# Kernel optimization log

Hardware: AMD Instinct MI355X
Metric: run time of the kernel (lower is better)

The kernel has to match this reference:

```python
import jax, jax.numpy as jnp
import numpy as np

K = 5
P = 1.5
MU = 0.01
N_NODES = 100000
N_EDGES = 1600000
D_FEAT = 32


def setup_inputs() -> dict:
    key = jax.random.key(0)
    k1, k2 = jax.random.split(key)
    h = jax.random.normal(k1, (N_NODES, D_FEAT), dtype=jnp.float32)
    edge_index = jax.random.randint(k2, (2, N_EDGES), 0, N_NODES, dtype=jnp.int64)
    return {"h": h, "edge_index": edge_index}


def reference(h, edge_index):
    row, col = edge_index[0], edge_index[1]
    for _ in range(K):
        diff = h[row] - h[col]                      # [E, d] gather
        norm_diff = jnp.maximum(jnp.linalg.norm(diff, axis=1), 1e-6)  # [E]
        weights = (norm_diff / norm_diff.max()) ** (P - 2.0)          # [E]
        # agg[r] += sum over edges with row==r of weights * (h[col] - h[row])
        msgs = weights[:, None] * (-diff)           # [E, d]
        agg = jax.ops.segment_sum(msgs, row, num_segments=N_NODES)    # [N, d]
        h = h - MU * agg
    return h
```

## Files before the change

kernel.cpp:

```cpp
#include <hip/hip_runtime.h>

#define NN 100000
#define NE 1600000
#define DF 32
#define KIT 5
#define MU 0.01f
#define NSLOT 256
#define NV4 (NN * DF / 4)
#define ELLW 36
#define AUXCAP 65536
#define NSLICE 8
#define SLICEN (NN / NSLICE)


__global__ __launch_bounds__(256) void zero_kernel(int* __restrict__ p, int n) {
    int i = blockIdx.x * blockDim.x + threadIdx.x;
    if (i < n) p[i] = 0;
}

__global__ __launch_bounds__(256) void ell_fill_kernel(const int* __restrict__ row,
                                                       const int* __restrict__ col,
                                                       int* __restrict__ degc,
                                                       int* __restrict__ colell,
                                                       int* __restrict__ auxcnt,
                                                       int2* __restrict__ aux) {
    const int slice = blockIdx.x & (NSLICE - 1);
    const int group = blockIdx.x >> 3;
    const int ngroups = gridDim.x >> 3;
    const int lo = slice * SLICEN;
    const int hi = lo + SLICEN;
    for (int e = group * 256 + (int)threadIdx.x; e < NE; e += ngroups * 256) {
        const int r = row[e];
        if (r >= lo && r < hi) {
            const int c = col[e];
            const int pos = atomicAdd(&degc[r], 1);
            if (pos < ELLW) {
                colell[r * ELLW + pos] = c;
            } else {
                const int a = atomicAdd(auxcnt, 1);
                if (a < AUXCAP) aux[a] = make_int2(r, c);
            }
        }
    }
}


__device__ __forceinline__ unsigned int pack2bf(float a, float b) {
    unsigned int ua = __float_as_uint(a);
    unsigned int ub = __float_as_uint(b);
    return ((ua + 0x8000u) >> 16) | (((ub + 0x8000u) >> 16) << 16);
}

__device__ __forceinline__ void unpack8(uint4 v, float* f) {
    f[0] = __uint_as_float(v.x << 16);
    f[1] = __uint_as_float(v.x & 0xffff0000u);
    f[2] = __uint_as_float(v.y << 16);
    f[3] = __uint_as_float(v.y & 0xffff0000u);
    f[4] = __uint_as_float(v.z << 16);
    f[5] = __uint_as_float(v.z & 0xffff0000u);
    f[6] = __uint_as_float(v.w << 16);
    f[7] = __uint_as_float(v.w & 0xffff0000u);
}

__global__ __launch_bounds__(256) void tobf16_kernel(const float4* __restrict__ h,
                                                     uint2* __restrict__ hb) {
    int i = blockIdx.x * blockDim.x + threadIdx.x;
    if (i < NV4) {
        const float4 v = h[i];
        hb[i] = make_uint2(pack2bf(v.x, v.y), pack2bf(v.z, v.w));
    }
}


__global__ __launch_bounds__(256) void agg_kernel(const uint4* __restrict__ hb4,
                                                  const int* __restrict__ degc,
                                                  const int* __restrict__ colell,
                                                  float* __restrict__ S,
                                                  int* __restrict__ maxslots) {
    const int lane = threadIdx.x & 31;
    const int q = lane >> 2;
    const int f2 = lane & 3;
    const int pair = (blockIdx.x * blockDim.x + threadIdx.x) >> 5;
    const int n0 = pair * 2;
    const int n1 = n0 + 1;

    const int d0 = min(degc[n0], ELLW);
    const int d1 = min(degc[n1], ELLW);

    const int ca = (lane < d0) ? colell[n0 * ELLW + lane] : n0;
    const int cb = (lane < d1) ? colell[n1 * ELLW + lane] : n1;
    const uint4 hru0 = hb4[n0 * 4 + f2];
    const uint4 hru1 = hb4[n1 * 4 + f2];

    uint4 u0[4], u1[4];
    #pragma unroll
    for (int j = 0; j < 4; ++j) u0[j] = hb4[__shfl(ca, 8 * j + q, 32) * 4 + f2];
    #pragma unroll
    for (int j = 0; j < 4; ++j) u1[j] = hb4[__shfl(cb, 8 * j + q, 32) * 4 + f2];

    float hr0[8], hr1[8];
    unpack8(hru0, hr0);
    unpack8(hru1, hr1);

    float acc0[8], acc1[8];
    #pragma unroll
    for (int i = 0; i < 8; ++i) { acc0[i] = 0.0f; acc1[i] = 0.0f; }
    float nmax = 0.0f;

    #pragma unroll
    for (int j = 0; j < 4; ++j) {
        float d[8];
        unpack8(u0[j], d);
        float s = 0.0f;
        #pragma unroll
        for (int i = 0; i < 8; ++i) {
            d[i] = hr0[i] - d[i];
            s = fmaf(d[i], d[i], s);
        }
        s += __shfl_xor(s, 1, 32);
        s += __shfl_xor(s, 2, 32);
        const float n = fmaxf(sqrtf(s), 1e-6f);
        nmax = fmaxf(nmax, n);
        const float w = rsqrtf(n);
        #pragma unroll
        for (int i = 0; i < 8; ++i) acc0[i] = fmaf(-d[i], w, acc0[i]);
    }
    #pragma unroll
    for (int j = 0; j < 4; ++j) {
        float d[8];
        unpack8(u1[j], d);
        float s = 0.0f;
        #pragma unroll
        for (int i = 0; i < 8; ++i) {
            d[i] = hr1[i] - d[i];
            s = fmaf(d[i], d[i], s);
        }
        s += __shfl_xor(s, 1, 32);
        s += __shfl_xor(s, 2, 32);
        const float n = fmaxf(sqrtf(s), 1e-6f);
        nmax = fmaxf(nmax, n);
        const float w = rsqrtf(n);
        #pragma unroll
        for (int i = 0; i < 8; ++i) acc1[i] = fmaf(-d[i], w, acc1[i]);
    }

    for (int k = 32; k < d0; k += 8) {
        const int ei = k + q;
        const int c = (ei < d0) ? colell[n0 * ELLW + ei] : n0;
        const uint4 uu = hb4[c * 4 + f2];
        float d[8];
        unpack8(uu, d);
        float s = 0.0f;
        #pragma unroll
        for (int i = 0; i < 8; ++i) {
            d[i] = hr0[i] - d[i];
            s = fmaf(d[i], d[i], s);
        }
        s += __shfl_xor(s, 1, 32);
        s += __shfl_xor(s, 2, 32);
        const float n = fmaxf(sqrtf(s), 1e-6f);
        nmax = fmaxf(nmax, n);
        const float w = rsqrtf(n);
        #pragma unroll
        for (int i = 0; i < 8; ++i) acc0[i] = fmaf(-d[i], w, acc0[i]);
    }
    for (int k = 32; k < d1; k += 8) {
        const int ei = k + q;
        const int c = (ei < d1) ? colell[n1 * ELLW + ei] : n1;
        const uint4 uu = hb4[c * 4 + f2];
        float d[8];
        unpack8(uu, d);
        float s = 0.0f;
        #pragma unroll
        for (int i = 0; i < 8; ++i) {
            d[i] = hr1[i] - d[i];
            s = fmaf(d[i], d[i], s);
        }
        s += __shfl_xor(s, 1, 32);
        s += __shfl_xor(s, 2, 32);
        const float n = fmaxf(sqrtf(s), 1e-6f);
        nmax = fmaxf(nmax, n);
        const float w = rsqrtf(n);
        #pragma unroll
        for (int i = 0; i < 8; ++i) acc1[i] = fmaf(-d[i], w, acc1[i]);
    }

    #pragma unroll
    for (int m = 4; m < 32; m <<= 1) {
        #pragma unroll
        for (int i = 0; i < 8; ++i) {
            acc0[i] += __shfl_xor(acc0[i], m, 32);
            acc1[i] += __shfl_xor(acc1[i], m, 32);
        }
    }
    if (q == 0) {
        ((float4*)S)[n0 * 8 + f2 * 2] = make_float4(acc0[0], acc0[1], acc0[2], acc0[3]);
        ((float4*)S)[n0 * 8 + f2 * 2 + 1] = make_float4(acc0[4], acc0[5], acc0[6], acc0[7]);
        ((float4*)S)[n1 * 8 + f2 * 2] = make_float4(acc1[0], acc1[1], acc1[2], acc1[3]);
        ((float4*)S)[n1 * 8 + f2 * 2 + 1] = make_float4(acc1[4], acc1[5], acc1[6], acc1[7]);
    }

    nmax = fmaxf(nmax, __shfl_xor(nmax, 4, 32));
    nmax = fmaxf(nmax, __shfl_xor(nmax, 8, 32));
    nmax = fmaxf(nmax, __shfl_xor(nmax, 16, 32));
    nmax = fmaxf(nmax, __shfl_xor(nmax, 32, 64));
    if ((threadIdx.x & 63) == 0) {
        atomicMax(&maxslots[blockIdx.x & (NSLOT - 1)], __float_as_int(nmax));
    }
}

__global__ __launch_bounds__(256) void aux_kernel(const uint2* __restrict__ hb,
                                                  const int2* __restrict__ aux,
                                                  const int* __restrict__ auxcnt,
                                                  float* __restrict__ S,
                                                  int* __restrict__ maxslots) {
    const int n = min(*auxcnt, AUXCAP);
    for (int i = blockIdx.x * blockDim.x + threadIdx.x; i < n;
         i += gridDim.x * blockDim.x) {
        const int r = aux[i].x;
        const int c = aux[i].y;
        float d[32];
        float s = 0.0f;
        for (int j = 0; j < 8; ++j) {
            const uint2 ur = hb[r * 8 + j];
            const uint2 uc = hb[c * 8 + j];
            float fr[4], fc[4];
            fr[0] = __uint_as_float(ur.x << 16);
            fr[1] = __uint_as_float(ur.x & 0xffff0000u);
            fr[2] = __uint_as_float(ur.y << 16);
            fr[3] = __uint_as_float(ur.y & 0xffff0000u);
            fc[0] = __uint_as_float(uc.x << 16);
            fc[1] = __uint_as_float(uc.x & 0xffff0000u);
            fc[2] = __uint_as_float(uc.y << 16);
            fc[3] = __uint_as_float(uc.y & 0xffff0000u);
            #pragma unroll
            for (int k = 0; k < 4; ++k) {
                d[j * 4 + k] = fr[k] - fc[k];
                s = fmaf(d[j * 4 + k], d[j * 4 + k], s);
            }
        }
        const float nn = fmaxf(sqrtf(s), 1e-6f);
        atomicMax(&maxslots[i & (NSLOT - 1)], __float_as_int(nn));
        const float w = rsqrtf(nn);
        for (int f = 0; f < 32; ++f) atomicAdd(&S[r * DF + f], -d[f] * w);
    }
}

__global__ __launch_bounds__(256) void update_kernel(const float4* __restrict__ hcur,
                                                     float4* __restrict__ hnxt,
                                                     uint2* __restrict__ hb,
                                                     const float4* __restrict__ S,
                                                     const int* __restrict__ slots) {
    const int t = threadIdx.x;
    int v = slots[t];
    #pragma unroll
    for (int m = 32; m > 0; m >>= 1) v = max(v, __shfl_xor(v, m, 64));
    __shared__ int sm[4];
    __shared__ float sscale;
    if ((t & 63) == 0) sm[t >> 6] = v;
    __syncthreads();
    if (t == 0) {
        int bm = max(max(sm[0], sm[1]), max(sm[2], sm[3]));
        sscale = MU * sqrtf(__int_as_float(bm));
    }
    __syncthreads();
    const float scale = sscale;
    const int i = blockIdx.x * blockDim.x + t;
    if (i < NV4) {
        const float4 hv = hcur[i];
        const float4 sv = S[i];
        float4 o;
        o.x = hv.x - scale * sv.x;
        o.y = hv.y - scale * sv.y;
        o.z = hv.z - scale * sv.z;
        o.w = hv.w - scale * sv.w;
        hnxt[i] = o;
        hb[i] = make_uint2(pack2bf(o.x, o.y), pack2bf(o.z, o.w));
    }
}

extern "C" void kernel_launch(void* const* d_in, const int* in_sizes, int n_in,
                              void* d_out, int out_size, void* d_ws, size_t ws_size,
                              hipStream_t stream) {
    const float* h_in = (const float*)d_in[0];
    const int* row = (const int*)d_in[1];
    const int* col = row + NE;
    float* out = (float*)d_out;

    float* S = (float*)d_ws;
    int* maxslots = (int*)(S + NN * DF);
    int* degc = maxslots + KIT * NSLOT;
    int* auxcnt = degc + NN;
    uintptr_t pa = (uintptr_t)(auxcnt + 1);
    pa = (pa + 7) & ~(uintptr_t)7;
    int2* aux = (int2*)pa;
    int* colell = (int*)(aux + AUXCAP);
    uintptr_t p = (uintptr_t)(colell + NN * ELLW);
    p = (p + 15) & ~(uintptr_t)15;
    uint2* hb = (uint2*)p;

    const int zb = (NN + 1 + 255) / 256;
    const int fb = NSLICE * 256;
    const int gb = (NN / 2 * 32 + 255) / 256;
    const int ub = (NV4 + 255) / 256;

    zero_kernel<<<zb, 256, 0, stream>>>(degc, NN + 1);
    ell_fill_kernel<<<fb, 256, 0, stream>>>(row, col, degc, colell, auxcnt, aux);
    tobf16_kernel<<<ub, 256, 0, stream>>>((const float4*)h_in, hb);

    for (int it = 0; it < KIT; ++it) {
        const float* cur = (it == 0) ? h_in : out;
        agg_kernel<<<gb, 256, 0, stream>>>((const uint4*)hb, degc, colell, S,
                                           maxslots + it * NSLOT);
        aux_kernel<<<32, 256, 0, stream>>>(hb, aux, auxcnt, S, maxslots + it * NSLOT);
        update_kernel<<<ub, 256, 0, stream>>>((const float4*)cur, (float4*)out, hb,
                                              (const float4*)S,
                                              maxslots + it * NSLOT);
    }
}
```

Before: 406.0 us.

## Add bucket-partition pass for ELL build and use nontemporal loads/stores

The ELL build is split in two. A first pass partitions edges into per-slice buckets with wave ballots and block-local prefix sums, and a second pass reads only the edges for its own slice. Before, each slice re-scanned the whole edge list. Separately, streaming loads and stores in the bf16 conversion, aggregation and update kernels are switched to nontemporal variants to reduce cache pollution. This adds an extra kernel launch and reuses the S buffer as bucket scratch, and edges that overflow a 64-entry bucket segment are sent to the aux path, which uses atomics.

```diff
diff --git a/kernel.cpp b/kernel.cpp
--- a/kernel.cpp
+++ b/kernel.cpp
@@ -11,6 +11,10 @@
 #define AUXCAP 65536
 #define NSLICE 8
 #define SLICEN (NN / NSLICE)
+#define NBLKA (NE / 256)
+#define SEGW 64
+
+typedef float f32x4 __attribute__((ext_vector_type(4)));
 
 
 __global__ __launch_bounds__(256) void zero_kernel(int* __restrict__ p, int n) {
@@ -18,21 +22,72 @@
     if (i < n) p[i] = 0;
 }
 
-__global__ __launch_bounds__(256) void ell_fill_kernel(const int* __restrict__ row,
+__global__ __launch_bounds__(256) void ell_part_kernel(const int* __restrict__ row,
                                                        const int* __restrict__ col,
+                                                       unsigned int* __restrict__ buck,
+                                                       int* __restrict__ cnts,
+                                                       int* __restrict__ auxcnt,
+                                                       int2* __restrict__ aux) {
+    __shared__ int wcnt[4][8];
+    __shared__ int woff[4][8];
+    const int t = threadIdx.x;
+    const int w = t >> 6;
+    const int lane = t & 63;
+    const int e = blockIdx.x * 256 + t;
+    const int r = __builtin_nontemporal_load(&row[e]);
+    const int c = __builtin_nontemporal_load(&col[e]);
+    const int b = r / SLICEN;
+    const int rl = r - b * SLICEN;
+    const unsigned int packed = ((unsigned int)rl << 17) | (unsigned int)c;
+
+    int myprefix = 0;
+    #pragma unroll
+    for (int k = 0; k < 8; ++k) {
+        const unsigned long long mk = __ballot(b == k);
+        if (lane == 0) wcnt[w][k] = __popcll(mk);
+        if (k == b) myprefix = __popcll(mk & ((1ull << lane) - 1ull));
+    }
+    __syncthreads();
+    if (t < 32) {
+        const int w2 = t >> 3, k = t & 7;
+        int o = 0;
+        for (int w3 = 0; w3 < w2; ++w3) o += wcnt[w3][k];
+        woff[w2][k] = o;
+    }
+    if (t < 8) {
+        cnts[blockIdx.x * 8 + t] = wcnt[0][t] + wcnt[1][t] + wcnt[2][t] + wcnt[3][t];
+    }
+    __syncthreads();
+
+    const int pos = woff[w][b] + myprefix;
+    if (pos < SEGW) {
+        buck[(b * NBLKA + (int)blockIdx.x) * SEGW + pos] = packed;
+    } else {
+        const int a = atomicAdd(auxcnt, 1);
+        if (a < AUXCAP) aux[a] = make_int2(r, c);
+    }
+}
+
+__global__ __launch_bounds__(256) void ell_fill_kernel(const unsigned int* __restrict__ buck,
+                                                       const int* __restrict__ cnts,
                                                        int* __restrict__ degc,
                                                        int* __restrict__ colell,
                                                        int* __restrict__ auxcnt,
                                                        int2* __restrict__ aux) {
-    const int slice = blockIdx.x & (NSLICE - 1);
-    const int group = blockIdx.x >> 3;
-    const int ngroups = gridDim.x >> 3;
-    const int lo = slice * SLICEN;
-    const int hi = lo + SLICEN;
-    for (int e = group * 256 + (int)threadIdx.x; e < NE; e += ngroups * 256) {
-        const int r = row[e];
-        if (r >= lo && r < hi) {
-            const int c = col[e];
+    const int s = blockIdx.x & (NSLICE - 1);
+    const int g = blockIdx.x >> 3;
+    const int ng = gridDim.x >> 3;
+    const int t = threadIdx.x;
+    const int j = t & 63;
+    const int bo = t >> 6;
+    const int lo = s * SLICEN;
+    for (int blk = g * 4 + bo; blk < NBLKA; blk += ng * 4) {
+        const int cnt = min(cnts[blk * 8 + s], SEGW);
+        if (j < cnt) {
+            const unsigned int pk =
+                __builtin_nontemporal_load(&buck[(s * NBLKA + blk) * SEGW + j]);
+            const int c = (int)(pk & 0x1ffffu);
+            const int r = lo + (int)(pk >> 17);
             const int pos = atomicAdd(&degc[r], 1);
             if (pos < ELLW) {
                 colell[r * ELLW + pos] = c;
@@ -62,11 +117,16 @@
     f[7] = __uint_as_float(v.w & 0xffff0000u);
 }
 
-__global__ __launch_bounds__(256) void tobf16_kernel(const float4* __restrict__ h,
+__device__ __forceinline__ void nt_store4(float* p, float a, float b, float c, float d) {
+    f32x4 v = {a, b, c, d};
+    __builtin_nontemporal_store(v, (f32x4*)p);
+}
+
+__global__ __launch_bounds__(256) void tobf16_kernel(const float* __restrict__ h,
                                                      uint2* __restrict__ hb) {
     int i = blockIdx.x * blockDim.x + threadIdx.x;
     if (i < NV4) {
-        const float4 v = h[i];
+        const f32x4 v = __builtin_nontemporal_load(((const f32x4*)h) + i);
         hb[i] = make_uint2(pack2bf(v.x, v.y), pack2bf(v.z, v.w));
     }
 }
@@ -87,8 +147,8 @@
     const int d0 = min(degc[n0], ELLW);
     const int d1 = min(degc[n1], ELLW);
 
-    const int ca = (lane < d0) ? colell[n0 * ELLW + lane] : n0;
-    const int cb = (lane < d1) ? colell[n1 * ELLW + lane] : n1;
+    const int ca = (lane < d0) ? __builtin_nontemporal_load(&colell[n0 * ELLW + lane]) : n0;
+    const int cb = (lane < d1) ? __builtin_nontemporal_load(&colell[n1 * ELLW + lane]) : n1;
     const uint4 hru0 = hb4[n0 * 4 + f2];
     const uint4 hru1 = hb4[n1 * 4 + f2];
 
@@ -146,7 +206,7 @@
 
     for (int k = 32; k < d0; k += 8) {
         const int ei = k + q;
-        const int c = (ei < d0) ? colell[n0 * ELLW + ei] : n0;
+        const int c = (ei < d0) ? __builtin_nontemporal_load(&colell[n0 * ELLW + ei]) : n0;
         const uint4 uu = hb4[c * 4 + f2];
         float d[8];
         unpack8(uu, d);
@@ -166,7 +226,7 @@
     }
     for (int k = 32; k < d1; k += 8) {
         const int ei = k + q;
-        const int c = (ei < d1) ? colell[n1 * ELLW + ei] : n1;
+        const int c = (ei < d1) ? __builtin_nontemporal_load(&colell[n1 * ELLW + ei]) : n1;
         const uint4 uu = hb4[c * 4 + f2];
         float d[8];
         unpack8(uu, d);
@@ -194,10 +254,10 @@
         }
     }
     if (q == 0) {
-        ((float4*)S)[n0 * 8 + f2 * 2] = make_float4(acc0[0], acc0[1], acc0[2], acc0[3]);
-        ((float4*)S)[n0 * 8 + f2 * 2 + 1] = make_float4(acc0[4], acc0[5], acc0[6], acc0[7]);
-        ((float4*)S)[n1 * 8 + f2 * 2] = make_float4(acc1[0], acc1[1], acc1[2], acc1[3]);
-        ((float4*)S)[n1 * 8 + f2 * 2 + 1] = make_float4(acc1[4], acc1[5], acc1[6], acc1[7]);
+        nt_store4(S + n0 * 32 + f2 * 8,     acc0[0], acc0[1], acc0[2], acc0[3]);
+        nt_store4(S + n0 * 32 + f2 * 8 + 4, acc0[4], acc0[5], acc0[6], acc0[7]);
+        nt_store4(S + n1 * 32 + f2 * 8,     acc1[0], acc1[1], acc1[2], acc1[3]);
+        nt_store4(S + n1 * 32 + f2 * 8 + 4, acc1[4], acc1[5], acc1[6], acc1[7]);
     }
 
     nmax = fmaxf(nmax, __shfl_xor(nmax, 4, 32));
@@ -246,10 +306,10 @@
     }
 }
 
-__global__ __launch_bounds__(256) void update_kernel(const float4* __restrict__ hcur,
-                                                     float4* __restrict__ hnxt,
+__global__ __launch_bounds__(256) void update_kernel(const float* __restrict__ hcur,
+                                                     float* __restrict__ hnxt,
                                                      uint2* __restrict__ hb,
-                                                     const float4* __restrict__ S,
+                                                     const float* __restrict__ S,
                                                      const int* __restrict__ slots) {
     const int t = threadIdx.x;
     int v = slots[t];
@@ -267,14 +327,10 @@
     const float scale = sscale;
     const int i = blockIdx.x * blockDim.x + t;
     if (i < NV4) {
-        const float4 hv = hcur[i];
-        const float4 sv = S[i];
-        float4 o;
-        o.x = hv.x - scale * sv.x;
-        o.y = hv.y - scale * sv.y;
-        o.z = hv.z - scale * sv.z;
-        o.w = hv.w - scale * sv.w;
-        hnxt[i] = o;
+        const f32x4 hv = __builtin_nontemporal_load(((const f32x4*)hcur) + i);
+        const f32x4 sv = __builtin_nontemporal_load(((const f32x4*)S) + i);
+        const f32x4 o = hv - scale * sv;
+        __builtin_nontemporal_store(o, ((f32x4*)hnxt) + i);
         hb[i] = make_uint2(pack2bf(o.x, o.y), pack2bf(o.z, o.w));
     }
 }
@@ -298,6 +354,8 @@
     uintptr_t p = (uintptr_t)(colell + NN * ELLW);
     p = (p + 15) & ~(uintptr_t)15;
     uint2* hb = (uint2*)p;
+    int* cnts = (int*)(hb + NV4);
+    unsigned int* buck = (unsigned int*)S;
 
     const int zb = (NN + 1 + 255) / 256;
     const int fb = NSLICE * 256;
@@ -305,16 +363,16 @@
     const int ub = (NV4 + 255) / 256;
 
     zero_kernel<<<zb, 256, 0, stream>>>(degc, NN + 1);
-    ell_fill_kernel<<<fb, 256, 0, stream>>>(row, col, degc, colell, auxcnt, aux);
-    tobf16_kernel<<<ub, 256, 0, stream>>>((const float4*)h_in, hb);
+    ell_part_kernel<<<NBLKA, 256, 0, stream>>>(row, col, buck, cnts, auxcnt, aux);
+    ell_fill_kernel<<<fb, 256, 0, stream>>>(buck, cnts, degc, colell, auxcnt, aux);
+    tobf16_kernel<<<ub, 256, 0, stream>>>(h_in, hb);
 
     for (int it = 0; it < KIT; ++it) {
         const float* cur = (it == 0) ? h_in : out;
         agg_kernel<<<gb, 256, 0, stream>>>((const uint4*)hb, degc, colell, S,
                                            maxslots + it * NSLOT);
         aux_kernel<<<32, 256, 0, stream>>>(hb, aux, auxcnt, S, maxslots + it * NSLOT);
-        update_kernel<<<ub, 256, 0, stream>>>((const float4*)cur, (float4*)out, hb,
-                                              (const float4*)S,
+        update_kernel<<<ub, 256, 0, stream>>>(cur, out, hb, (const float*)S,
                                               maxslots + it * NSLOT);
     }
 }
```

Measured after the change: 435.1 us. 7.2% more time.
